# Kernel tuning notes

Hardware: AMD Instinct MI355X
Metric: run time of the kernel (lower is better)

## Reference

```python
import jax, jax.numpy as jnp
import numpy as np

NUM_HEADS = 16
NUM_KV_HEADS = 4
HEAD_DIM = 128
LAYER_IDX = 5
MASK_VALUE = -65504.0  # torch.finfo(torch.float16).min


def setup_inputs() -> dict:
    key = jax.random.key(0)
    ks = jax.random.split(key, 7)
    B, S, H = 2, 2048, 2048
    hidden_states = jax.random.normal(ks[0], (B, S, H), dtype=jnp.float32)
    k = jax.random.normal(ks[1], (B, NUM_KV_HEADS, S, HEAD_DIM), dtype=jnp.float32)
    v = jax.random.normal(ks[2], (B, NUM_KV_HEADS, S, HEAD_DIM), dtype=jnp.float32)
    std = 0.02
    w_q = jax.random.normal(ks[3], (H, H), dtype=jnp.float32) * std
    b_q = jnp.zeros((H,), dtype=jnp.float32)
    w_proj = jax.random.normal(ks[4], (H, H), dtype=jnp.float32) * (std / np.sqrt(2 * 24))
    b_proj = jnp.zeros((H,), dtype=jnp.float32)
    return {"hidden_states": hidden_states, "key": k, "value": v,
            "w_q": w_q, "b_q": b_q, "w_proj": w_proj, "b_proj": b_proj}


def reference(hidden_states, key, value, w_q, b_q, w_proj, b_proj):
    B, S, H = hidden_states.shape
    G = NUM_HEADS // NUM_KV_HEADS  # query heads per kv head
    dtype = hidden_states.dtype

    # query projection -> [B, kv_heads, group, S, head_dim]
    q = hidden_states @ w_q.T + b_q
    q = q.reshape(B, S, NUM_KV_HEADS, G, HEAD_DIM).transpose(0, 2, 3, 1, 4)

    # bigcode-style fp32 softmax with layer-wise unscale
    unscale = float(LAYER_IDX + 1)  # scale_attention_softmax_in_fp32 and upcast
    scale_factor = (1.0 / unscale) * (HEAD_DIM ** -0.5)  # scale_attn_weights

    # scores: [B, kv_heads, group, S_q, S_k]
    scores = jnp.einsum('bkgsd,bktd->bkgst', q, key) * scale_factor

    causal = jnp.tril(jnp.ones((S, S), dtype=bool))  # [S_q, S_k]
    scores = jnp.where(causal, scores, jnp.asarray(MASK_VALUE, dtype=scores.dtype))

    probs = jax.nn.softmax((scores * unscale).astype(jnp.float32), axis=-1).astype(dtype)

    out = jnp.einsum('bkgst,bktd->bkgsd', probs, value)
    out = out.transpose(0, 3, 1, 2, 4).reshape(B, S, H)
    out = out @ w_proj.T + b_proj
    return out
```

## Files before the change

### kernel.cpp

```cpp
#include <hip/hip_runtime.h>
#include <math.h>


#define RSQ128 0.08838834764831845f
#define MASK6  (-393024.0f)

typedef __attribute__((ext_vector_type(8))) short short8;
typedef __attribute__((ext_vector_type(4))) float f32x4;

static __device__ __forceinline__ unsigned short f2bf(float x) {
    union { float f; unsigned u; } v; v.f = x;
    unsigned r = v.u + 0x7FFFu + ((v.u >> 16) & 1u);
    return (unsigned short)(r >> 16);
}

static __device__ __forceinline__ void gl_lds16(const void* g, void* l) {
    __builtin_amdgcn_global_load_lds(
        (const __attribute__((address_space(1))) void*)g,
        (__attribute__((address_space(3))) void*)l, 16, 0, 0);
}

__global__ void cvt_bf16(const float* __restrict__ in, unsigned short* __restrict__ out) {
    const int i = (blockIdx.x * 256 + threadIdx.x) * 8;
    const float4 a = *(const float4*)(in + i);
    const float4 b = *(const float4*)(in + i + 4);
    short8 o;
    o[0] = (short)f2bf(a.x); o[1] = (short)f2bf(a.y);
    o[2] = (short)f2bf(a.z); o[3] = (short)f2bf(a.w);
    o[4] = (short)f2bf(b.x); o[5] = (short)f2bf(b.y);
    o[6] = (short)f2bf(b.z); o[7] = (short)f2bf(b.w);
    *(short8*)(out + i) = o;
}

__global__ void vtrans_bf16(const float* __restrict__ V, unsigned short* __restrict__ Vt) {
    __shared__ float Ts[64][65];
    const int t = threadIdx.x;
    const int s0 = blockIdx.x * 64, d0 = blockIdx.y * 64;
    const float* src = V + (size_t)blockIdx.z * 2048 * 128;
    unsigned short* dst = Vt + (size_t)blockIdx.z * 128 * 2048;
#pragma unroll
    for (int p = 0; p < 4; ++p) {
        const int f = p * 256 + t, r = f >> 4, cq = f & 15;
        const float4 v = *(const float4*)(src + (size_t)(s0 + r) * 128 + d0 + cq * 4);
        Ts[r][cq * 4 + 0] = v.x; Ts[r][cq * 4 + 1] = v.y;
        Ts[r][cq * 4 + 2] = v.z; Ts[r][cq * 4 + 3] = v.w;
    }
    __syncthreads();
#pragma unroll
    for (int p = 0; p < 2; ++p) {
        const int f = p * 256 + t, dr = f >> 3, c = f & 7;
        short8 o;
#pragma unroll
        for (int j = 0; j < 8; ++j) o[j] = (short)f2bf(Ts[c * 8 + j][dr]);
        *(short8*)(dst + (size_t)(d0 + dr) * 2048 + s0 + c * 8) = o;
    }
}

template <bool BF16OUT>
__global__ __launch_bounds__(256, 2) void gemm_nt_mfma(
    const unsigned short* __restrict__ A,
    const unsigned short* __restrict__ W,
    const float* __restrict__ bias,
    void* __restrict__ Cout, int M, int N, int K)
{
    __shared__ __align__(16) unsigned short As[128 * 32];
    __shared__ __align__(16) unsigned short Ws[128 * 32];
    const int tid = threadIdx.x, lane = tid & 63, w = tid >> 6;
    const int wm = w & 1, wn = w >> 1;
    const int m0 = blockIdx.y * 128, n0 = blockIdx.x * 128;
    const int r0 = tid >> 2, c0 = tid & 3;

    const unsigned short* Ag = A + (size_t)(m0 + r0) * K + c0 * 8;
    const unsigned short* Wg = W + (size_t)(n0 + r0) * K + c0 * 8;

    f32x4 acc[4][4];
#pragma unroll
    for (int i = 0; i < 4; ++i)
#pragma unroll
        for (int j = 0; j < 4; ++j) acc[i][j] = (f32x4){0.f, 0.f, 0.f, 0.f};

    const int lm = lane & 15, lk = (lane >> 4) * 8;

    for (int k0 = 0; k0 < K; k0 += 32) {
        __syncthreads();
        gl_lds16(Ag + k0,                 As + tid * 8);
        gl_lds16(Ag + (size_t)64 * K + k0, As + (tid + 256) * 8);
        gl_lds16(Wg + k0,                 Ws + tid * 8);
        gl_lds16(Wg + (size_t)64 * K + k0, Ws + (tid + 256) * 8);
        __syncthreads();

        short8 a[4], b[4];
#pragma unroll
        for (int i = 0; i < 4; ++i)
            a[i] = *(const short8*)&As[(64 * wm + 16 * i + lm) * 32 + lk];
#pragma unroll
        for (int j = 0; j < 4; ++j)
            b[j] = *(const short8*)&Ws[(64 * wn + 16 * j + lm) * 32 + lk];
#pragma unroll
        for (int i = 0; i < 4; ++i)
#pragma unroll
            for (int j = 0; j < 4; ++j)
                acc[i][j] = __builtin_amdgcn_mfma_f32_16x16x32_bf16(a[i], b[j], acc[i][j], 0, 0, 0);
    }

    float bv[4];
#pragma unroll
    for (int j = 0; j < 4; ++j) bv[j] = bias[n0 + 64 * wn + 16 * j + lm];
#pragma unroll
    for (int i = 0; i < 4; ++i)
#pragma unroll
        for (int reg = 0; reg < 4; ++reg) {
            const int row = m0 + 64 * wm + 16 * i + 4 * (lane >> 4) + reg;
#pragma unroll
            for (int j = 0; j < 4; ++j) {
                const int col = n0 + 64 * wn + 16 * j + lm;
                const float v = acc[i][j][reg] + bv[j];
                if (BF16OUT) ((unsigned short*)Cout)[(size_t)row * N + col] = f2bf(v);
                else         ((float*)Cout)[(size_t)row * N + col] = v;
            }
        }
}

__global__ __launch_bounds__(256, 2) void attn_mfma(
    const unsigned short* __restrict__ Q,
    const unsigned short* __restrict__ Kg_,
    const unsigned short* __restrict__ Vt,
    unsigned short* __restrict__ O)
{
    __shared__ __align__(16) unsigned short Qs[64 * 128];
    __shared__ __align__(16) unsigned short Ks[64 * 128];
    __shared__ __align__(16) unsigned short Vs[128 * 64];
    __shared__ __align__(16) unsigned short Ps[64 * 64];

    const int tid = threadIdx.x, lane = tid & 63, w = tid >> 6;
    const int bid = blockIdx.x;
    const int qb = 31 - (bid >> 5);
    const int bh = bid & 31;
    const int s0 = qb * 64;
    const int b = bh >> 4, h = bh & 15, kh = h >> 2;

    const unsigned short* Qg = Q + (size_t)(b * 2048 + s0) * 2048 + h * 128;
    const unsigned short* Kb = Kg_ + (size_t)(b * 4 + kh) * 2048 * 128;
    const unsigned short* Vg = Vt + (size_t)(b * 4 + kh) * 128 * 2048;

#pragma unroll
    for (int p = 0; p < 4; ++p) {
        const int f = p * 256 + tid, r = f >> 4, c = f & 15;
        const short8 v = *(const short8*)(Qg + (size_t)r * 2048 + c * 8);
        *(short8*)&Qs[(r * 16 + (c ^ (r & 15))) * 8] = v;
    }

    f32x4 aO[8];
#pragma unroll
    for (int nt = 0; nt < 8; ++nt) aO[nt] = (f32x4){0.f, 0.f, 0.f, 0.f};
    float m_[4], l_[4];
#pragma unroll
    for (int r = 0; r < 4; ++r) { m_[r] = -INFINITY; l_[r] = 0.f; }

    const int lm = lane & 15;
    const int lg = lane >> 4;

    for (int t0 = 0; t0 <= s0; t0 += 64) {
        __syncthreads();
#pragma unroll
        for (int p = 0; p < 4; ++p) {
            const int f = p * 256 + tid, r = f >> 4, c = f & 15;
            const short8 v = *(const short8*)(Kb + (size_t)(t0 + r) * 128 + c * 8);
            *(short8*)&Ks[(r * 16 + (c ^ (r & 15))) * 8] = v;
        }
#pragma unroll
        for (int p = 0; p < 4; ++p) {
            const int f = p * 256 + tid, d = f >> 3, c = f & 7;
            const short8 v = *(const short8*)(Vg + (size_t)d * 2048 + t0 + c * 8);
            *(short8*)&Vs[(d * 8 + (c ^ (d & 7))) * 8] = v;
        }
        __syncthreads();

        f32x4 s4[4];
#pragma unroll
        for (int jt = 0; jt < 4; ++jt) s4[jt] = (f32x4){0.f, 0.f, 0.f, 0.f};
#pragma unroll
        for (int k0 = 0; k0 < 128; k0 += 32) {
            const int ca = (k0 >> 3) + lg;
            const int mq = 16 * w + lm;
            const short8 a = *(const short8*)&Qs[(mq * 16 + (ca ^ (mq & 15))) * 8];
#pragma unroll
            for (int jt = 0; jt < 4; ++jt) {
                const int nk = 16 * jt + lm;
                const short8 bf = *(const short8*)&Ks[(nk * 16 + (ca ^ (nk & 15))) * 8];
                s4[jt] = __builtin_amdgcn_mfma_f32_16x16x32_bf16(a, bf, s4[jt], 0, 0, 0);
            }
        }

        float pm[4];
#pragma unroll
        for (int r = 0; r < 4; ++r) {
            const int ql = 16 * w + 4 * lg + r;
            float mx = -1e30f;
#pragma unroll
            for (int jt = 0; jt < 4; ++jt) {
                const int kl = 16 * jt + lm;
                const float v = (t0 + kl > s0 + ql) ? MASK6 : s4[jt][r] * RSQ128;
                s4[jt][r] = v;
                mx = fmaxf(mx, v);
            }
            pm[r] = mx;
        }
#pragma unroll
        for (int off = 1; off < 16; off <<= 1)
#pragma unroll
            for (int r = 0; r < 4; ++r)
                pm[r] = fmaxf(pm[r], __shfl_xor(pm[r], off, 16));

        float al[4];
#pragma unroll
        for (int r = 0; r < 4; ++r) {
            const float mn = fmaxf(m_[r], pm[r]);
            al[r] = __expf(m_[r] - mn);
            m_[r] = mn;
        }
#pragma unroll
        for (int nt = 0; nt < 8; ++nt)
#pragma unroll
            for (int r = 0; r < 4; ++r) aO[nt][r] *= al[r];

        float ls[4];
#pragma unroll
        for (int r = 0; r < 4; ++r) {
            const int q = 16 * w + 4 * lg + r;
            float s = 0.f;
#pragma unroll
            for (int jt = 0; jt < 4; ++jt) {
                const float p = __expf(s4[jt][r] - m_[r]);
                s += p;
                const int key = 16 * jt + lm;
                Ps[q * 64 + ((key >> 3) ^ (q & 7)) * 8 + (key & 7)] = f2bf(p);
            }
            ls[r] = s;
        }
#pragma unroll
        for (int off = 1; off < 16; off <<= 1)
#pragma unroll
            for (int r = 0; r < 4; ++r) ls[r] += __shfl_xor(ls[r], off, 16);
#pragma unroll
        for (int r = 0; r < 4; ++r) l_[r] = l_[r] * al[r] + ls[r];

        __syncthreads();

#pragma unroll
        for (int k0 = 0; k0 < 64; k0 += 32) {
            const int ca = (k0 >> 3) + lg;
            const int mq = 16 * w + lm;
            const short8 a = *(const short8*)&Ps[(mq * 8 + (ca ^ (mq & 7))) * 8];
#pragma unroll
            for (int nt = 0; nt < 8; ++nt) {
                const int nd = 16 * nt + lm;
                const short8 bf = *(const short8*)&Vs[(nd * 8 + (ca ^ (nd & 7))) * 8];
                aO[nt] = __builtin_amdgcn_mfma_f32_16x16x32_bf16(a, bf, aO[nt], 0, 0, 0);
            }
        }
    }

#pragma unroll
    for (int r = 0; r < 4; ++r) {
        const float inv = 1.0f / l_[r];
        const int row = s0 + 16 * w + 4 * lg + r;
        unsigned short* op = O + (size_t)(b * 2048 + row) * 2048 + h * 128;
#pragma unroll
        for (int nt = 0; nt < 8; ++nt)
            op[16 * nt + lm] = f2bf(aO[nt][r] * inv);
    }
}

extern "C" void kernel_launch(void* const* d_in, const int* in_sizes, int n_in,
                              void* d_out, int out_size, void* d_ws, size_t ws_size,
                              hipStream_t stream) {
    const float* hs = (const float*)d_in[0];
    const float* k  = (const float*)d_in[1];
    const float* v  = (const float*)d_in[2];
    const float* wq = (const float*)d_in[3];
    const float* bq = (const float*)d_in[4];
    const float* wp = (const float*)d_in[5];
    const float* bp = (const float*)d_in[6];
    float* out = (float*)d_out;

    unsigned short* hsb  = (unsigned short*)d_ws;
    unsigned short* wqb  = hsb  + 8388608;
    unsigned short* kb   = wqb  + 4194304;
    unsigned short* vtb  = kb   + 2097152;
    unsigned short* qbuf = vtb  + 2097152;
    unsigned short* abuf = qbuf + 8388608;
    unsigned short* wpb  = hsb;

    cvt_bf16<<<4096, 256, 0, stream>>>(hs, hsb);
    cvt_bf16<<<2048, 256, 0, stream>>>(wq, wqb);
    cvt_bf16<<<1024, 256, 0, stream>>>(k, kb);
    vtrans_bf16<<<dim3(32, 2, 8), 256, 0, stream>>>(v, vtb);

    dim3 gG(16, 32);
    gemm_nt_mfma<true><<<gG, 256, 0, stream>>>(hsb, wqb, bq, qbuf, 4096, 2048, 2048);
    cvt_bf16<<<2048, 256, 0, stream>>>(wp, wpb);
    attn_mfma<<<1024, 256, 0, stream>>>(qbuf, kb, vtb, abuf);
    gemm_nt_mfma<false><<<gG, 256, 0, stream>>>(abuf, wpb, bp, out, 4096, 2048, 2048);
}
```

Measured before the change: 323.8 us.

## Rewrite attention with 32x32 MFMA, register-resident Q and P, 128-row tiles

```diff
diff --git a/kernel.cpp b/kernel.cpp
--- a/kernel.cpp
+++ b/kernel.cpp
@@ -7,6 +7,7 @@
 
 typedef __attribute__((ext_vector_type(8))) short short8;
 typedef __attribute__((ext_vector_type(4))) float f32x4;
+typedef __attribute__((ext_vector_type(16))) float f32x16;
 
 static __device__ __forceinline__ unsigned short f2bf(float x) {
     union { float f; unsigned u; } v; v.f = x;
@@ -83,9 +84,9 @@
 
     for (int k0 = 0; k0 < K; k0 += 32) {
         __syncthreads();
-        gl_lds16(Ag + k0,                 As + tid * 8);
+        gl_lds16(Ag + k0,                  As + tid * 8);
         gl_lds16(Ag + (size_t)64 * K + k0, As + (tid + 256) * 8);
-        gl_lds16(Wg + k0,                 Ws + tid * 8);
+        gl_lds16(Wg + k0,                  Ws + tid * 8);
         gl_lds16(Wg + (size_t)64 * K + k0, Ws + (tid + 256) * 8);
         __syncthreads();
 
@@ -121,46 +122,44 @@
         }
 }
 
-__global__ __launch_bounds__(256, 2) void attn_mfma(
+__global__ __launch_bounds__(256, 2) void attn_mfma2(
     const unsigned short* __restrict__ Q,
     const unsigned short* __restrict__ Kg_,
     const unsigned short* __restrict__ Vt,
     unsigned short* __restrict__ O)
 {
-    __shared__ __align__(16) unsigned short Qs[64 * 128];
     __shared__ __align__(16) unsigned short Ks[64 * 128];
     __shared__ __align__(16) unsigned short Vs[128 * 64];
-    __shared__ __align__(16) unsigned short Ps[64 * 64];
 
     const int tid = threadIdx.x, lane = tid & 63, w = tid >> 6;
+    const int h2 = lane >> 5;
+    const int ln = lane & 31;
+
     const int bid = blockIdx.x;
-    const int qb = 31 - (bid >> 5);
+    const int jj = bid >> 5;
+    const int qb = (jj < 8) ? (15 - jj) : (jj - 8);
     const int bh = bid & 31;
-    const int s0 = qb * 64;
+    const int s0 = qb * 128;
     const int b = bh >> 4, h = bh & 15, kh = h >> 2;
 
-    const unsigned short* Qg = Q + (size_t)(b * 2048 + s0) * 2048 + h * 128;
     const unsigned short* Kb = Kg_ + (size_t)(b * 4 + kh) * 2048 * 128;
     const unsigned short* Vg = Vt + (size_t)(b * 4 + kh) * 128 * 2048;
 
-#pragma unroll
-    for (int p = 0; p < 4; ++p) {
-        const int f = p * 256 + tid, r = f >> 4, c = f & 15;
-        const short8 v = *(const short8*)(Qg + (size_t)r * 2048 + c * 8);
-        *(short8*)&Qs[(r * 16 + (c ^ (r & 15))) * 8] = v;
-    }
-
-    f32x4 aO[8];
-#pragma unroll
-    for (int nt = 0; nt < 8; ++nt) aO[nt] = (f32x4){0.f, 0.f, 0.f, 0.f};
-    float m_[4], l_[4];
-#pragma unroll
-    for (int r = 0; r < 4; ++r) { m_[r] = -INFINITY; l_[r] = 0.f; }
-
-    const int lm = lane & 15;
-    const int lg = lane >> 4;
-
-    for (int t0 = 0; t0 <= s0; t0 += 64) {
+    const int qg = s0 + 32 * w + ln;
+    const unsigned short* Qp = Q + (size_t)(b * 2048 + qg) * 2048 + h * 128 + h2 * 8;
+    short8 Qreg[8];
+#pragma unroll
+    for (int ks = 0; ks < 8; ++ks) Qreg[ks] = *(const short8*)(Qp + ks * 16);
+
+    f32x16 Ot[4];
+#pragma unroll
+    for (int mt = 0; mt < 4; ++mt)
+#pragma unroll
+        for (int r = 0; r < 16; ++r) Ot[mt][r] = 0.f;
+    float m_ = -INFINITY, l_ = 0.f;
+
+    const int tmax = s0 + 64;
+    for (int t0 = 0; t0 <= tmax; t0 += 64) {
         __syncthreads();
 #pragma unroll
         for (int p = 0; p < 4; ++p) {
@@ -176,99 +175,95 @@
         }
         __syncthreads();
 
-        f32x4 s4[4];
-#pragma unroll
-        for (int jt = 0; jt < 4; ++jt) s4[jt] = (f32x4){0.f, 0.f, 0.f, 0.f};
-#pragma unroll
-        for (int k0 = 0; k0 < 128; k0 += 32) {
-            const int ca = (k0 >> 3) + lg;
-            const int mq = 16 * w + lm;
-            const short8 a = *(const short8*)&Qs[(mq * 16 + (ca ^ (mq & 15))) * 8];
-#pragma unroll
-            for (int jt = 0; jt < 4; ++jt) {
-                const int nk = 16 * jt + lm;
-                const short8 bf = *(const short8*)&Ks[(nk * 16 + (ca ^ (nk & 15))) * 8];
-                s4[jt] = __builtin_amdgcn_mfma_f32_16x16x32_bf16(a, bf, s4[jt], 0, 0, 0);
+        if (t0 <= s0 + 32 * w + 31) {
+            f32x16 St[2];
+#pragma unroll
+            for (int kt = 0; kt < 2; ++kt)
+#pragma unroll
+                for (int r = 0; r < 16; ++r) St[kt][r] = 0.f;
+#pragma unroll
+            for (int ks = 0; ks < 8; ++ks)
+#pragma unroll
+                for (int kt = 0; kt < 2; ++kt) {
+                    const int key = 32 * kt + ln;
+                    const int ch = (2 * ks + h2) ^ (key & 15);
+                    const short8 a = *(const short8*)&Ks[(key * 16 + ch) * 8];
+                    St[kt] = __builtin_amdgcn_mfma_f32_32x32x16_bf16(a, Qreg[ks], St[kt], 0, 0, 0);
+                }
+
+            float mx = -INFINITY;
+#pragma unroll
+            for (int kt = 0; kt < 2; ++kt)
+#pragma unroll
+                for (int r = 0; r < 16; ++r) {
+                    const int key = t0 + 32 * kt + (r & 3) + 8 * (r >> 2) + 4 * h2;
+                    const float v = (key <= qg) ? St[kt][r] * RSQ128 : MASK6;
+                    St[kt][r] = v;
+                    mx = fmaxf(mx, v);
+                }
+            mx = fmaxf(mx, __shfl_xor(mx, 32));
+            const float mn = fmaxf(m_, mx);
+            const float alpha = __expf(m_ - mn);
+            m_ = mn;
+
+            float s_loc = 0.f;
+            unsigned Pp[16];
+#pragma unroll
+            for (int kt = 0; kt < 2; ++kt)
+#pragma unroll
+                for (int p = 0; p < 8; ++p) {
+                    const float p0 = __expf(St[kt][2 * p] - mn);
+                    const float p1 = __expf(St[kt][2 * p + 1] - mn);
+                    s_loc += p0 + p1;
+                    Pp[kt * 8 + p] = (unsigned)f2bf(p0) | ((unsigned)f2bf(p1) << 16);
+                }
+            s_loc += __shfl_xor(s_loc, 32);
+            l_ = l_ * alpha + s_loc;
+#pragma unroll
+            for (int mt = 0; mt < 4; ++mt)
+#pragma unroll
+                for (int r = 0; r < 16; ++r) Ot[mt][r] *= alpha;
+
+#pragma unroll
+            for (int ks4 = 0; ks4 < 4; ++ks4) {
+                const int base = (ks4 >> 1) * 8 + 4 * (ks4 & 1);
+                const unsigned pa = Pp[base + 0], pb = Pp[base + 1];
+                const unsigned pc = Pp[base + 2], pd = Pp[base + 3];
+                const unsigned x0 = (unsigned)__shfl_xor((int)(h2 ? pa : pc), 32);
+                const unsigned x1 = (unsigned)__shfl_xor((int)(h2 ? pb : pd), 32);
+                union { unsigned u[4]; short8 s8; } fr;
+                fr.u[0] = h2 ? x0 : pa;
+                fr.u[1] = h2 ? x1 : pb;
+                fr.u[2] = h2 ? pc : x0;
+                fr.u[3] = h2 ? pd : x1;
+#pragma unroll
+                for (int mt = 0; mt < 4; ++mt) {
+                    const int d = 32 * mt + ln;
+                    const int ch = (2 * ks4 + h2) ^ (d & 7);
+                    const short8 a = *(const short8*)&Vs[(d * 8 + ch) * 8];
+                    Ot[mt] = __builtin_amdgcn_mfma_f32_32x32x16_bf16(a, fr.s8, Ot[mt], 0, 0, 0);
+                }
             }
         }
-
-        float pm[4];
-#pragma unroll
-        for (int r = 0; r < 4; ++r) {
-            const int ql = 16 * w + 4 * lg + r;
-            float mx = -1e30f;
-#pragma unroll
-            for (int jt = 0; jt < 4; ++jt) {
-                const int kl = 16 * jt + lm;
-                const float v = (t0 + kl > s0 + ql) ? MASK6 : s4[jt][r] * RSQ128;
-                s4[jt][r] = v;
-                mx = fmaxf(mx, v);
-            }
-            pm[r] = mx;
-        }
-#pragma unroll
-        for (int off = 1; off < 16; off <<= 1)
-#pragma unroll
-            for (int r = 0; r < 4; ++r)
-                pm[r] = fmaxf(pm[r], __shfl_xor(pm[r], off, 16));
-
-        float al[4];
-#pragma unroll
-        for (int r = 0; r < 4; ++r) {
-            const float mn = fmaxf(m_[r], pm[r]);
-            al[r] = __expf(m_[r] - mn);
-            m_[r] = mn;
-        }
-#pragma unroll
-        for (int nt = 0; nt < 8; ++nt)
-#pragma unroll
-            for (int r = 0; r < 4; ++r) aO[nt][r] *= al[r];
-
-        float ls[4];
-#pragma unroll
-        for (int r = 0; r < 4; ++r) {
-            const int q = 16 * w + 4 * lg + r;
-            float s = 0.f;
-#pragma unroll
-            for (int jt = 0; jt < 4; ++jt) {
-                const float p = __expf(s4[jt][r] - m_[r]);
-                s += p;
-                const int key = 16 * jt + lm;
-                Ps[q * 64 + ((key >> 3) ^ (q & 7)) * 8 + (key & 7)] = f2bf(p);
-            }
-            ls[r] = s;
-        }
-#pragma unroll
-        for (int off = 1; off < 16; off <<= 1)
-#pragma unroll
-            for (int r = 0; r < 4; ++r) ls[r] += __shfl_xor(ls[r], off, 16);
-#pragma unroll
-        for (int r = 0; r < 4; ++r) l_[r] = l_[r] * al[r] + ls[r];
-
-        __syncthreads();
-
-#pragma unroll
-        for (int k0 = 0; k0 < 64; k0 += 32) {
-            const int ca = (k0 >> 3) + lg;
-            const int mq = 16 * w + lm;
-            const short8 a = *(const short8*)&Ps[(mq * 8 + (ca ^ (mq & 7))) * 8];
-#pragma unroll
-            for (int nt = 0; nt < 8; ++nt) {
-                const int nd = 16 * nt + lm;
-                const short8 bf = *(const short8*)&Vs[(nd * 8 + (ca ^ (nd & 7))) * 8];
-                aO[nt] = __builtin_amdgcn_mfma_f32_16x16x32_bf16(a, bf, aO[nt], 0, 0, 0);
-            }
-        }
-    }
-
-#pragma unroll
-    for (int r = 0; r < 4; ++r) {
-        const float inv = 1.0f / l_[r];
-        const int row = s0 + 16 * w + 4 * lg + r;
-        unsigned short* op = O + (size_t)(b * 2048 + row) * 2048 + h * 128;
-#pragma unroll
-        for (int nt = 0; nt < 8; ++nt)
-            op[16 * nt + lm] = f2bf(aO[nt][r] * inv);
+    }
+
+    __syncthreads();
+    unsigned short* Es = ((w & 2) ? Vs : Ks) + (w & 1) * 4096;
+    const float inv = 1.0f / l_;
+#pragma unroll
+    for (int mt = 0; mt < 4; ++mt)
+#pragma unroll
+        for (int r = 0; r < 16; ++r) {
+            const int d = 32 * mt + (r & 3) + 8 * (r >> 2) + 4 * h2;
+            Es[ln * 128 + (((d >> 3) ^ (ln & 15)) * 8) + (d & 7)] = f2bf(Ot[mt][r] * inv);
+        }
+    __syncthreads();
+#pragma unroll
+    for (int pp = 0; pp < 8; ++pp) {
+        const int f = pp * 64 + lane;
+        const int q = f >> 4, c = f & 15;
+        const short8 v = *(const short8*)&Es[q * 128 + ((c ^ (q & 15)) * 8)];
+        *(short8*)(O + (size_t)(b * 2048 + s0 + 32 * w + q) * 2048 + h * 128 + c * 8) = v;
     }
 }
 
@@ -300,6 +295,6 @@
     dim3 gG(16, 32);
     gemm_nt_mfma<true><<<gG, 256, 0, stream>>>(hsb, wqb, bq, qbuf, 4096, 2048, 2048);
     cvt_bf16<<<2048, 256, 0, stream>>>(wp, wpb);
-    attn_mfma<<<1024, 256, 0, stream>>>(qbuf, kb, vtb, abuf);
+    attn_mfma2<<<512, 256, 0, stream>>>(qbuf, kb, vtb, abuf);
     gemm_nt_mfma<false><<<gG, 256, 0, stream>>>(abuf, wpb, bp, out, 4096, 2048, 2048);
 }
```

Measured after the change: 357.1 us. 10.3% more time.
